# Kernel optimization log

Measured on AMD Instinct MI355X. Metric: run time of the kernel, lower is better.

The kernel has to match this reference:

```python
import jax, jax.numpy as jnp
import numpy as np

DIM = 256
WIN = (2, 7, 7)
NH = 8
BW = 2048  # num_windows * batch
N_TOK = WIN[0] * WIN[1] * WIN[2]  # 98


def _rel_coords_table():
    # Swin-V2 continuous log-spaced relative coordinates table, flattened to [T, 3]
    d = np.arange(-(WIN[0] - 1), WIN[0], dtype=np.float32)
    h = np.arange(-(WIN[1] - 1), WIN[1], dtype=np.float32)
    w = np.arange(-(WIN[2] - 1), WIN[2], dtype=np.float32)
    g = np.stack(np.meshgrid(d, h, w, indexing='ij'), axis=-1)  # [2Wd-1, 2Wh-1, 2Ww-1, 3]
    eps = 1e-6
    g[..., 0] /= WIN[0] - (1 - eps)
    g[..., 1] /= WIN[1] - (1 - eps)
    g[..., 2] /= WIN[2] - (1 - eps)
    g *= 8.0
    g = np.sign(g) * np.log2(np.abs(g) + 1.0) / np.log2(8.0)
    return g.reshape(-1, 3).astype(np.float32)


def _rel_pos_index():
    # integer relative position index [N, N] into the flattened table
    coords = np.stack(np.meshgrid(np.arange(WIN[0]), np.arange(WIN[1]), np.arange(WIN[2]), indexing='ij'))
    cf = coords.reshape(3, -1)
    rc = (cf[:, :, None] - cf[:, None, :]).transpose(1, 2, 0)
    rc[..., 0] += WIN[0] - 1
    rc[..., 1] += WIN[1] - 1
    rc[..., 2] += WIN[2] - 1
    rc[..., 0] *= (2 * WIN[1] - 1) * (2 * WIN[2] - 1)
    rc[..., 1] *= 2 * WIN[2] - 1
    return rc.sum(-1).astype(np.int32)  # [N, N]


def setup_inputs() -> dict:
    key = jax.random.key(0)
    ks = jax.random.split(key, 6)
    x = jax.random.normal(ks[0], (BW, N_TOK, DIM), dtype=jnp.float32)
    qkv_w = jax.random.normal(ks[1], (3 * DIM, DIM), dtype=jnp.float32) * 0.02
    q_bias = jnp.zeros((DIM,), dtype=jnp.float32)
    v_bias = jnp.zeros((DIM,), dtype=jnp.float32)
    logit_scale = jnp.log(10.0) * jnp.ones((NH, 1, 1), dtype=jnp.float32)
    cpb_w1 = jax.random.normal(ks[2], (512, 3), dtype=jnp.float32) * 0.02
    cpb_b1 = jnp.zeros((512,), dtype=jnp.float32)
    cpb_w2 = jax.random.normal(ks[3], (NH, 512), dtype=jnp.float32) * 0.02
    proj_w = jax.random.normal(ks[4], (DIM, DIM), dtype=jnp.float32) * 0.02
    proj_b = jnp.zeros((DIM,), dtype=jnp.float32)
    return {"x": x, "qkv_w": qkv_w, "q_bias": q_bias, "v_bias": v_bias,
            "logit_scale": logit_scale, "cpb_w1": cpb_w1, "cpb_b1": cpb_b1,
            "cpb_w2": cpb_w2, "proj_w": proj_w, "proj_b": proj_b}


def reference(x, qkv_w, q_bias, v_bias, logit_scale, cpb_w1, cpb_b1, cpb_w2, proj_w, proj_b):
    B_, N, C = x.shape
    hd = C // NH
    # qkv with separate q/v biases and zero k bias (Swin-V2)
    bias = jnp.concatenate([q_bias, jnp.zeros_like(q_bias), v_bias])
    qkv = (x @ qkv_w.T + bias).reshape(B_, N, 3, NH, hd).transpose(2, 0, 3, 1, 4)
    q, k, v = qkv[0], qkv[1], qkv[2]  # each [B_, NH, N, hd]
    # cosine attention: L2-normalize q, k (F.normalize eps=1e-12)
    qn = q / jnp.maximum(jnp.linalg.norm(q, axis=-1, keepdims=True), 1e-12)
    kn = k / jnp.maximum(jnp.linalg.norm(k, axis=-1, keepdims=True), 1e-12)
    attn = jnp.einsum('bhnd,bhmd->bhnm', qn, kn)
    scale = jnp.exp(jnp.minimum(logit_scale, jnp.log(jnp.float32(100.0))))  # clamp at log(1/0.01)
    attn = attn * scale  # [NH,1,1] broadcasts
    # continuous relative position bias via cpb MLP
    table = jnp.asarray(_rel_coords_table())                     # [T, 3]
    bt = jax.nn.relu(table @ cpb_w1.T + cpb_b1) @ cpb_w2.T       # [T, NH]
    idx = jnp.asarray(_rel_pos_index().reshape(-1))              # [N*N]
    rpb = bt[idx].reshape(N, N, NH).transpose(2, 0, 1)           # [NH, N, N]
    rpb = 16.0 * jax.nn.sigmoid(rpb)
    attn = jax.nn.softmax(attn + rpb[None], axis=-1)
    out = jnp.einsum('bhnm,bhmd->bhnd', attn, v).transpose(0, 2, 1, 3).reshape(B_, N, C)
    return out @ proj_w.T + proj_b
```

## Files before the change

kernel.cpp:

```cpp
#include <hip/hip_runtime.h>
#include <math.h>

typedef _Float16 f16;
typedef _Float16 f16x4 __attribute__((ext_vector_type(4)));
typedef _Float16 f16x8 __attribute__((ext_vector_type(8)));
typedef float f32x4 __attribute__((ext_vector_type(4)));

#define NTOK 98
#define BWIN 2048

#define OFF_BT    0u
#define OFF_RPB   (1u<<20)
#define OFF_WQKV  (2u<<20)
#define OFF_WPROJ (3u<<20)
#define OFF_Q     (4u<<20)
#define QKV_SZ    (2048u*8u*98u*32u*2u)
#define OFF_K     (OFF_Q + QKV_SZ)
#define OFF_V     (OFF_K + QKV_SZ)
#define OFF_AV    (OFF_V + QKV_SZ)

__device__ __forceinline__ void gload16(const f16* g, f16* l) {
  __builtin_amdgcn_global_load_lds(
      (const __attribute__((address_space(1))) void*)g,
      (__attribute__((address_space(3))) void*)l, 16, 0, 0);
}
__device__ __forceinline__ void gload16f(const float* g, float* l) {
  __builtin_amdgcn_global_load_lds(
      (const __attribute__((address_space(1))) void*)g,
      (__attribute__((address_space(3))) void*)l, 16, 0, 0);
}

__global__ void prep_bt(const float* __restrict__ w1, const float* __restrict__ b1,
                        const float* __restrict__ w2, float* __restrict__ bt) {
  int t = blockIdx.x;
  int lane = threadIdx.x;
  int a = t / 169, rem = t % 169, b = rem / 13, c = rem % 13;
  float g0 = ((float)(a - 1) / 1.000001f) * 8.0f;
  float g1 = ((float)(b - 6) / 6.000001f) * 8.0f;
  float g2 = ((float)(c - 6) / 6.000001f) * 8.0f;
  float t0 = log2f(fabsf(g0) + 1.0f) / 3.0f; t0 = (g0 < 0.f) ? -t0 : t0;
  float t1 = log2f(fabsf(g1) + 1.0f) / 3.0f; t1 = (g1 < 0.f) ? -t1 : t1;
  float t2 = log2f(fabsf(g2) + 1.0f) / 3.0f; t2 = (g2 < 0.f) ? -t2 : t2;
  float part[8] = {0.f,0.f,0.f,0.f,0.f,0.f,0.f,0.f};
#pragma unroll
  for (int jj = 0; jj < 8; jj++) {
    int j = lane * 8 + jj;
    float hv = t0 * w1[j*3] + t1 * w1[j*3+1] + t2 * w1[j*3+2] + b1[j];
    hv = fmaxf(hv, 0.f);
#pragma unroll
    for (int h = 0; h < 8; h++) part[h] += hv * w2[h*512 + j];
  }
#pragma unroll
  for (int m = 1; m < 64; m <<= 1)
#pragma unroll
    for (int h = 0; h < 8; h++) part[h] += __shfl_xor(part[h], m);
  if (lane == 0)
#pragma unroll
    for (int h = 0; h < 8; h++) bt[t*8 + h] = part[h];
}

__global__ void prep_rpb(const float* __restrict__ bt, float* __restrict__ rpb) {
  int bid = blockIdx.x;
  int h = bid / 98, i = bid % 98;
  int j = threadIdx.x;
  if (j >= 112) return;
  float v = 0.f;
  if (j < 98) {
    int di = i / 49, hi = (i % 49) / 7, wi = i % 7;
    int dj = j / 49, hj = (j % 49) / 7, wj = j % 7;
    int idx = (di - dj + 1) * 169 + (hi - hj + 6) * 13 + (wi - wj + 6);
    float t = bt[idx*8 + h];
    v = 16.0f / (1.0f + expf(-t));
  }
  rpb[(h*98 + i)*112 + j] = v;
}

__global__ void prep_wt(const float* __restrict__ qkv_w, const float* __restrict__ proj_w,
                        f16* __restrict__ wq, f16* __restrict__ wp) {
  int t = blockIdx.x * 256 + threadIdx.x;
  wq[t] = (f16)qkv_w[t];
  if (t < 256*256) wp[t] = (f16)proj_w[t];
}

__global__ __launch_bounds__(256) void qkv_gemm(
    const float* __restrict__ x, const f16* __restrict__ wq,
    const float* __restrict__ q_bias, const float* __restrict__ v_bias,
    f16* __restrict__ qw, f16* __restrict__ kw, f16* __restrict__ vw) {
  __shared__ float Af0[128*32];
  __shared__ float Af1[128*32];
  __shared__ f16   Bf0[128*32];
  __shared__ f16   Bf1[128*32];
  int tid = threadIdx.x;
  int w = tid >> 6, lane = tid & 63, q4 = lane >> 4, l15 = lane & 15;

  int bid = blockIdx.x;
  int sid = (bid & 7) * 1176 + (bid >> 3);
  int n_t = sid % 6, m_t = sid / 6;
  int m0 = m_t * 128, n0 = n_t * 128;

  f32x4 acc[2][8] = {};

#define QSTAGE(AB, BB, KS)                                                     \
  {                                                                            \
    _Pragma("unroll")                                                          \
    for (int p = 0; p < 4; p++) {                                              \
      int e0 = p*256 + (w << 6);                                               \
      int e  = e0 + lane;                                                      \
      int r  = e >> 3, kc = e & 7;                                             \
      int kc2 = kc ^ ((r & 3) << 1);                                           \
      gload16f(x + (size_t)(m0 + r)*256 + (KS)*32 + kc2*4, &AB[e0*4]);         \
    }                                                                          \
    _Pragma("unroll")                                                          \
    for (int p = 0; p < 2; p++) {                                              \
      int e0 = p*256 + (w << 6);                                               \
      int e  = e0 + lane;                                                      \
      int r  = e >> 2, kc = e & 3;                                             \
      gload16(wq + (size_t)(n0 + r)*256 + (KS)*32 + kc*8, &BB[e0*8]);          \
    }                                                                          \
  }

#define QCOMPUTE(AB, BB)                                                       \
  {                                                                            \
    f16x8 af[2], bf[8];                                                        \
    _Pragma("unroll")                                                          \
    for (int mt = 0; mt < 2; mt++) {                                           \
      int row = w*32 + mt*16 + l15;                                            \
      int co = ((q4 ^ (row & 3)) << 3);                                        \
      f32x4 a0 = *(const f32x4*)(&AB[row*32 + co]);                            \
      f32x4 a1 = *(const f32x4*)(&AB[row*32 + co + 4]);                        \
      f16x8 v;                                                                 \
      v[0]=(f16)a0[0]; v[1]=(f16)a0[1]; v[2]=(f16)a0[2]; v[3]=(f16)a0[3];      \
      v[4]=(f16)a1[0]; v[5]=(f16)a1[1]; v[6]=(f16)a1[2]; v[7]=(f16)a1[3];      \
      af[mt] = v;                                                              \
    }                                                                          \
    _Pragma("unroll")                                                          \
    for (int nt = 0; nt < 8; nt++)                                             \
      bf[nt] = *(const f16x8*)(&BB[(nt*16 + l15)*32 + q4*8]);                  \
    _Pragma("unroll")                                                          \
    for (int mt = 0; mt < 2; mt++)                                             \
      _Pragma("unroll")                                                        \
      for (int nt = 0; nt < 8; nt++)                                           \
        acc[mt][nt] = __builtin_amdgcn_mfma_f32_16x16x32_f16(af[mt], bf[nt], acc[mt][nt], 0, 0, 0); \
  }

  QSTAGE(Af0, Bf0, 0)
  __syncthreads();
#pragma unroll
  for (int ks = 0; ks < 8; ks += 2) {
    QSTAGE(Af1, Bf1, ks + 1)
    QCOMPUTE(Af0, Bf0)
    __syncthreads();
    if (ks + 2 < 8) QSTAGE(Af0, Bf0, ks + 2)
    QCOMPUTE(Af1, Bf1)
    __syncthreads();
  }
#undef QSTAGE
#undef QCOMPUTE

  int s = n_t >> 1;
  f16* dst = (s == 0) ? qw : ((s == 1) ? kw : vw);
#pragma unroll
  for (int mt = 0; mt < 2; mt++)
#pragma unroll
    for (int nt = 0; nt < 8; nt++) {
      int c = n0 + nt*16 + l15;
      int hcol = (c >> 5) & 7, d = c & 31;
      float bias = (s == 0) ? q_bias[c & 255] : ((s == 2) ? v_bias[c & 255] : 0.0f);
#pragma unroll
      for (int r = 0; r < 4; r++) {
        int m = m0 + w*32 + mt*16 + q4*4 + r;
        int b = m / 98, tok = m % 98;
        dst[((size_t)(b*8 + hcol)*98 + tok)*32 + d] = (f16)(acc[mt][nt][r] + bias);
      }
    }
}

#define P_STR 136
__global__ __launch_bounds__(256) void attn_kernel(
    const f16* __restrict__ qw, const f16* __restrict__ kw, const f16* __restrict__ vw,
    const float* __restrict__ rpb, const float* __restrict__ logit_scale,
    f16* __restrict__ av) {
  __shared__ f16 Ps[4*16*P_STR];

  int tid = threadIdx.x;
  int wv = tid >> 6, lane = tid & 63, q4 = lane >> 4, l15 = lane & 15;
  int pair = blockIdx.x * 4 + wv;
  int b = pair >> 3, h = pair & 7;
  float scale = __expf(fminf(logit_scale[h], 4.6051701859880914f));
  const f16* qg = qw + ((size_t)pair) * (98*32);
  const f16* kg = kw + ((size_t)pair) * (98*32);
  const f16* vg = vw + ((size_t)pair) * (98*32);
  f16* pbuf = &Ps[wv * 16 * P_STR];

  {
    int r = lane >> 2, c0 = 112 + (lane & 3) * 4;
    *(ushort4*)(&pbuf[r*P_STR + c0]) = ushort4{0,0,0,0};
  }

  f16x8 kf[7];
#pragma unroll
  for (int nt = 0; nt < 7; nt++) {
    int row = nt*16 + l15; if (row > 97) row = 97;
    f16x8 raw = *(const f16x8*)(kg + row*32 + q4*8);
    float ss = 0.f;
#pragma unroll
    for (int j = 0; j < 8; j++) { float v = (float)raw[j]; ss = fmaf(v, v, ss); }
    ss += __shfl_xor(ss, 16);
    ss += __shfl_xor(ss, 32);
    float inv = 1.0f / fmaxf(sqrtf(ss), 1e-12f);
#pragma unroll
    for (int j = 0; j < 8; j++) kf[nt][j] = (f16)((float)raw[j] * inv);
  }

  f16x8 vf[2][4];
#pragma unroll
  for (int n = 0; n < 2; n++)
#pragma unroll
    for (int kt = 0; kt < 4; kt++)
#pragma unroll
      for (int j = 0; j < 8; j++) {
        int tok = kt*32 + q4*8 + j; if (tok > 97) tok = 97;
        vf[n][kt][j] = vg[tok*32 + n*16 + l15];
      }

  const float* rpb_h = rpb + (size_t)h * 98 * 112;

  for (int mt = 0; mt < 7; mt++) {
    int qrow = mt*16 + l15;
    int qcl = (qrow > 97) ? 97 : qrow;
    bool qv = qrow < 98;
    f16x8 qraw = *(const f16x8*)(qg + qcl*32 + q4*8);
    float ss = 0.f;
#pragma unroll
    for (int j = 0; j < 8; j++) { float v = (float)qraw[j]; ss = fmaf(v, v, ss); }
    ss += __shfl_xor(ss, 16);
    ss += __shfl_xor(ss, 32);
    float qinv = 1.0f / fmaxf(sqrtf(ss), 1e-12f);
    f16x8 aq;
#pragma unroll
    for (int j = 0; j < 8; j++) aq[j] = (f16)((float)qraw[j] * qinv);

    f32x4 lg[7];
    __builtin_amdgcn_s_setprio(1);
#pragma unroll
    for (int nt = 0; nt < 7; nt++) {
      f32x4 z = {0.f,0.f,0.f,0.f};
      lg[nt] = __builtin_amdgcn_mfma_f32_16x16x32_f16(kf[nt], aq, z, 0, 0, 0);
    }
    __builtin_amdgcn_s_setprio(0);

    float mrow = -1e30f;
#pragma unroll
    for (int nt = 0; nt < 7; nt++) {
      float4 rp = *(const float4*)(rpb_h + (size_t)qcl*112 + nt*16 + q4*4);
#pragma unroll
      for (int r = 0; r < 4; r++) {
        int k = nt*16 + q4*4 + r;
        float rv = (r == 0) ? rp.x : (r == 1) ? rp.y : (r == 2) ? rp.z : rp.w;
        float lv = (qv && k < 98) ? fmaf(scale, lg[nt][r], rv) : -1e30f;
        lg[nt][r] = lv;
        mrow = fmaxf(mrow, lv);
      }
    }
    mrow = fmaxf(mrow, __shfl_xor(mrow, 16));
    mrow = fmaxf(mrow, __shfl_xor(mrow, 32));
    float s = 0.f;
#pragma unroll
    for (int nt = 0; nt < 7; nt++)
#pragma unroll
      for (int r = 0; r < 4; r++) {
        float p = __expf(lg[nt][r] - mrow);
        lg[nt][r] = p;
        s += p;
      }
    s += __shfl_xor(s, 16);
    s += __shfl_xor(s, 32);
    float inv = 1.0f / s;
#pragma unroll
    for (int nt = 0; nt < 7; nt++) {
      f16x4 pv;
#pragma unroll
      for (int r = 0; r < 4; r++) pv[r] = (f16)(lg[nt][r] * inv);
      *(f16x4*)(&pbuf[l15*P_STR + nt*16 + q4*4]) = pv;
    }
    f16x8 pf[4];
#pragma unroll
    for (int kt = 0; kt < 4; kt++)
      pf[kt] = *(const f16x8*)(&pbuf[l15*P_STR + kt*32 + q4*8]);
    __builtin_amdgcn_s_setprio(1);
    f32x4 oacc[2];
#pragma unroll
    for (int n = 0; n < 2; n++) {
      f32x4 acc = {0.f,0.f,0.f,0.f};
#pragma unroll
      for (int kt = 0; kt < 4; kt++)
        acc = __builtin_amdgcn_mfma_f32_16x16x32_f16(pf[kt], vf[n][kt], acc, 0, 0, 0);
      oacc[n] = acc;
    }
    __builtin_amdgcn_s_setprio(0);
#pragma unroll
    for (int n = 0; n < 2; n++) {
      int d = n*16 + l15;
#pragma unroll
      for (int r = 0; r < 4; r++) {
        int row = mt*16 + q4*4 + r;
        if (row < 98)
          av[((size_t)(b*98 + row))*256 + h*32 + d] = (f16)oacc[n][r];
      }
    }
  }
}

__global__ __launch_bounds__(256) void proj_gemm(
    const f16* __restrict__ avi, const f16* __restrict__ wp,
    const float* __restrict__ pb, float* __restrict__ out) {
  __shared__ f16 Ap0[128*32];
  __shared__ f16 Ap1[128*32];
  __shared__ f16 Bp0[128*32];
  __shared__ f16 Bp1[128*32];
  int tid = threadIdx.x;
  int w = tid >> 6, lane = tid & 63, q4 = lane >> 4, l15 = lane & 15;

  int bid = blockIdx.x;
  int sid = (bid & 7) * 392 + (bid >> 3);
  int n_t = sid & 1, m_t = sid >> 1;
  int m0 = m_t * 128, n0 = n_t * 128;

  f32x4 acc[2][8] = {};

#define PSTAGE(AB, BB, KS)                                                     \
  {                                                                            \
    _Pragma("unroll")                                                          \
    for (int p = 0; p < 2; p++) {                                              \
      int e0 = p*256 + (w << 6);                                               \
      int e  = e0 + lane;                                                      \
      int r  = e >> 2, kc = e & 3;                                             \
      gload16(avi + (size_t)(m0 + r)*256 + (KS)*32 + kc*8, &AB[e0*8]);         \
      gload16(wp  + (size_t)(n0 + r)*256 + (KS)*32 + kc*8, &BB[e0*8]);         \
    }                                                                          \
  }

#define PCOMPUTE(AB, BB)                                                       \
  {                                                                            \
    f16x8 af[2], bf[8];                                                        \
    _Pragma("unroll")                                                          \
    for (int mt = 0; mt < 2; mt++)                                             \
      af[mt] = *(const f16x8*)(&AB[(w*32 + mt*16 + l15)*32 + q4*8]);           \
    _Pragma("unroll")                                                          \
    for (int nt = 0; nt < 8; nt++)                                             \
      bf[nt] = *(const f16x8*)(&BB[(nt*16 + l15)*32 + q4*8]);                  \
    _Pragma("unroll")                                                          \
    for (int mt = 0; mt < 2; mt++)                                             \
      _Pragma("unroll")                                                        \
      for (int nt = 0; nt < 8; nt++)                                           \
        acc[mt][nt] = __builtin_amdgcn_mfma_f32_16x16x32_f16(af[mt], bf[nt], acc[mt][nt], 0, 0, 0); \
  }

  PSTAGE(Ap0, Bp0, 0)
  __syncthreads();
#pragma unroll
  for (int ks = 0; ks < 8; ks += 2) {
    PSTAGE(Ap1, Bp1, ks + 1)
    PCOMPUTE(Ap0, Bp0)
    __syncthreads();
    if (ks + 2 < 8) PSTAGE(Ap0, Bp0, ks + 2)
    PCOMPUTE(Ap1, Bp1)
    __syncthreads();
  }
#undef PSTAGE
#undef PCOMPUTE

#pragma unroll
  for (int mt = 0; mt < 2; mt++)
#pragma unroll
    for (int nt = 0; nt < 8; nt++) {
      int c = n0 + nt*16 + l15;
      float bias = pb[c];
#pragma unroll
      for (int r = 0; r < 4; r++) {
        int m = m0 + w*32 + mt*16 + q4*4 + r;
        out[(size_t)m*256 + c] = acc[mt][nt][r] + bias;
      }
    }
}

extern "C" void kernel_launch(void* const* d_in, const int* in_sizes, int n_in,
                              void* d_out, int out_size, void* d_ws, size_t ws_size,
                              hipStream_t stream) {
  const float* x           = (const float*)d_in[0];
  const float* qkv_w       = (const float*)d_in[1];
  const float* q_bias      = (const float*)d_in[2];
  const float* v_bias      = (const float*)d_in[3];
  const float* logit_scale = (const float*)d_in[4];
  const float* cpb_w1      = (const float*)d_in[5];
  const float* cpb_b1      = (const float*)d_in[6];
  const float* cpb_w2      = (const float*)d_in[7];
  const float* proj_w      = (const float*)d_in[8];
  const float* proj_b      = (const float*)d_in[9];
  char* ws = (char*)d_ws;
  float* bt  = (float*)(ws + OFF_BT);
  float* rpb = (float*)(ws + OFF_RPB);
  f16* wq    = (f16*)(ws + OFF_WQKV);
  f16* wp    = (f16*)(ws + OFF_WPROJ);
  f16* qws   = (f16*)(ws + OFF_Q);
  f16* kws   = (f16*)(ws + OFF_K);
  f16* vws   = (f16*)(ws + OFF_V);
  f16* avs   = (f16*)(ws + OFF_AV);
  float* out = (float*)d_out;

  prep_bt<<<dim3(507), dim3(64), 0, stream>>>(cpb_w1, cpb_b1, cpb_w2, bt);
  prep_rpb<<<dim3(784), dim3(128), 0, stream>>>(bt, rpb);
  prep_wt<<<dim3(768), dim3(256), 0, stream>>>(qkv_w, proj_w, wq, wp);
  qkv_gemm<<<dim3(9408), dim3(256), 0, stream>>>(x, wq, q_bias, v_bias, qws, kws, vws);
  attn_kernel<<<dim3(4096), dim3(256), 0, stream>>>(qws, kws, vws, rpb, logit_scale, avs);
  proj_gemm<<<dim3(3136), dim3(256), 0, stream>>>(avs, wp, proj_b, out);
}
```

Baseline: 781.1 us.

## Triple-buffer LDS stages in QKV and projection GEMMs with explicit vmcnt waits

```diff
diff --git a/kernel.cpp b/kernel.cpp
--- a/kernel.cpp
+++ b/kernel.cpp
@@ -29,6 +29,9 @@
       (const __attribute__((address_space(1))) void*)g,
       (__attribute__((address_space(3))) void*)l, 16, 0, 0);
 }
+
+#define VMCNT(n) asm volatile("s_waitcnt vmcnt(" #n ")" ::: "memory")
+#define BAR() __builtin_amdgcn_s_barrier()
 
 __global__ void prep_bt(const float* __restrict__ w1, const float* __restrict__ b1,
                         const float* __restrict__ w2, float* __restrict__ bt) {
@@ -88,6 +91,7 @@
     f16* __restrict__ qw, f16* __restrict__ kw, f16* __restrict__ vw) {
   __shared__ float Af0[128*32];
   __shared__ float Af1[128*32];
+  __shared__ float Af2[128*32];
   __shared__ f16   Bf0[128*32];
   __shared__ f16   Bf1[128*32];
   int tid = threadIdx.x;
@@ -100,7 +104,7 @@
 
   f32x4 acc[2][8] = {};
 
-#define QSTAGE(AB, BB, KS)                                                     \
+#define QSTAGE_A(AB, KS)                                                       \
   {                                                                            \
     _Pragma("unroll")                                                          \
     for (int p = 0; p < 4; p++) {                                              \
@@ -110,6 +114,9 @@
       int kc2 = kc ^ ((r & 3) << 1);                                           \
       gload16f(x + (size_t)(m0 + r)*256 + (KS)*32 + kc2*4, &AB[e0*4]);         \
     }                                                                          \
+  }
+#define QSTAGE_B(BB, KS)                                                       \
+  {                                                                            \
     _Pragma("unroll")                                                          \
     for (int p = 0; p < 2; p++) {                                              \
       int e0 = p*256 + (w << 6);                                               \
@@ -119,7 +126,7 @@
     }                                                                          \
   }
 
-#define QCOMPUTE(AB, BB)                                                       \
+#define QPHASE(AB, BB, ...)                                                    \
   {                                                                            \
     f16x8 af[2], bf[8];                                                        \
     _Pragma("unroll")                                                          \
@@ -128,34 +135,44 @@
       int co = ((q4 ^ (row & 3)) << 3);                                        \
       f32x4 a0 = *(const f32x4*)(&AB[row*32 + co]);                            \
       f32x4 a1 = *(const f32x4*)(&AB[row*32 + co + 4]);                        \
-      f16x8 v;                                                                 \
-      v[0]=(f16)a0[0]; v[1]=(f16)a0[1]; v[2]=(f16)a0[2]; v[3]=(f16)a0[3];      \
-      v[4]=(f16)a1[0]; v[5]=(f16)a1[1]; v[6]=(f16)a1[2]; v[7]=(f16)a1[3];      \
-      af[mt] = v;                                                              \
+      f16x8 vv;                                                                \
+      vv[0]=(f16)a0[0]; vv[1]=(f16)a0[1]; vv[2]=(f16)a0[2]; vv[3]=(f16)a0[3];  \
+      vv[4]=(f16)a1[0]; vv[5]=(f16)a1[1]; vv[6]=(f16)a1[2]; vv[7]=(f16)a1[3];  \
+      af[mt] = vv;                                                             \
     }                                                                          \
     _Pragma("unroll")                                                          \
     for (int nt = 0; nt < 8; nt++)                                             \
       bf[nt] = *(const f16x8*)(&BB[(nt*16 + l15)*32 + q4*8]);                  \
+    __VA_ARGS__;                                                               \
+    __builtin_amdgcn_s_setprio(1);                                             \
     _Pragma("unroll")                                                          \
     for (int mt = 0; mt < 2; mt++)                                             \
       _Pragma("unroll")                                                        \
       for (int nt = 0; nt < 8; nt++)                                           \
         acc[mt][nt] = __builtin_amdgcn_mfma_f32_16x16x32_f16(af[mt], bf[nt], acc[mt][nt], 0, 0, 0); \
-  }
-
-  QSTAGE(Af0, Bf0, 0)
-  __syncthreads();
-#pragma unroll
-  for (int ks = 0; ks < 8; ks += 2) {
-    QSTAGE(Af1, Bf1, ks + 1)
-    QCOMPUTE(Af0, Bf0)
-    __syncthreads();
-    if (ks + 2 < 8) QSTAGE(Af0, Bf0, ks + 2)
-    QCOMPUTE(Af1, Bf1)
-    __syncthreads();
-  }
-#undef QSTAGE
-#undef QCOMPUTE
+    __builtin_amdgcn_s_setprio(0);                                             \
+  }
+
+  QSTAGE_A(Af0, 0) QSTAGE_B(Bf0, 0) QSTAGE_A(Af1, 1)
+  VMCNT(4); BAR();
+  QPHASE(Af0, Bf0, QSTAGE_B(Bf1, 1) QSTAGE_A(Af2, 2))
+  VMCNT(4); BAR();
+  QPHASE(Af1, Bf1, QSTAGE_B(Bf0, 2) QSTAGE_A(Af0, 3))
+  VMCNT(4); BAR();
+  QPHASE(Af2, Bf0, QSTAGE_B(Bf1, 3) QSTAGE_A(Af1, 4))
+  VMCNT(4); BAR();
+  QPHASE(Af0, Bf1, QSTAGE_B(Bf0, 4) QSTAGE_A(Af2, 5))
+  VMCNT(4); BAR();
+  QPHASE(Af1, Bf0, QSTAGE_B(Bf1, 5) QSTAGE_A(Af0, 6))
+  VMCNT(4); BAR();
+  QPHASE(Af2, Bf1, QSTAGE_B(Bf0, 6) QSTAGE_A(Af1, 7))
+  VMCNT(4); BAR();
+  QPHASE(Af0, Bf0, QSTAGE_B(Bf1, 7))
+  VMCNT(0); BAR();
+  QPHASE(Af1, Bf1, )
+#undef QSTAGE_A
+#undef QSTAGE_B
+#undef QPHASE
 
   int s = n_t >> 1;
   f16* dst = (s == 0) ? qw : ((s == 1) ? kw : vw);
@@ -316,8 +333,10 @@
     const float* __restrict__ pb, float* __restrict__ out) {
   __shared__ f16 Ap0[128*32];
   __shared__ f16 Ap1[128*32];
+  __shared__ f16 Ap2[128*32];
   __shared__ f16 Bp0[128*32];
   __shared__ f16 Bp1[128*32];
+  __shared__ f16 Bp2[128*32];
   int tid = threadIdx.x;
   int w = tid >> 6, lane = tid & 63, q4 = lane >> 4, l15 = lane & 15;
 
@@ -340,7 +359,7 @@
     }                                                                          \
   }
 
-#define PCOMPUTE(AB, BB)                                                       \
+#define PPHASE(AB, BB, ...)                                                    \
   {                                                                            \
     f16x8 af[2], bf[8];                                                        \
     _Pragma("unroll")                                                          \
@@ -349,26 +368,35 @@
     _Pragma("unroll")                                                          \
     for (int nt = 0; nt < 8; nt++)                                             \
       bf[nt] = *(const f16x8*)(&BB[(nt*16 + l15)*32 + q4*8]);                  \
+    __VA_ARGS__;                                                               \
+    __builtin_amdgcn_s_setprio(1);                                             \
     _Pragma("unroll")                                                          \
     for (int mt = 0; mt < 2; mt++)                                             \
       _Pragma("unroll")                                                        \
       for (int nt = 0; nt < 8; nt++)                                           \
         acc[mt][nt] = __builtin_amdgcn_mfma_f32_16x16x32_f16(af[mt], bf[nt], acc[mt][nt], 0, 0, 0); \
-  }
-
-  PSTAGE(Ap0, Bp0, 0)
-  __syncthreads();
-#pragma unroll
-  for (int ks = 0; ks < 8; ks += 2) {
-    PSTAGE(Ap1, Bp1, ks + 1)
-    PCOMPUTE(Ap0, Bp0)
-    __syncthreads();
-    if (ks + 2 < 8) PSTAGE(Ap0, Bp0, ks + 2)
-    PCOMPUTE(Ap1, Bp1)
-    __syncthreads();
-  }
+    __builtin_amdgcn_s_setprio(0);                                             \
+  }
+
+  PSTAGE(Ap0, Bp0, 0) PSTAGE(Ap1, Bp1, 1)
+  VMCNT(4); BAR();
+  PPHASE(Ap0, Bp0, PSTAGE(Ap2, Bp2, 2))
+  VMCNT(4); BAR();
+  PPHASE(Ap1, Bp1, PSTAGE(Ap0, Bp0, 3))
+  VMCNT(4); BAR();
+  PPHASE(Ap2, Bp2, PSTAGE(Ap1, Bp1, 4))
+  VMCNT(4); BAR();
+  PPHASE(Ap0, Bp0, PSTAGE(Ap2, Bp2, 5))
+  VMCNT(4); BAR();
+  PPHASE(Ap1, Bp1, PSTAGE(Ap0, Bp0, 6))
+  VMCNT(4); BAR();
+  PPHASE(Ap2, Bp2, PSTAGE(Ap1, Bp1, 7))
+  VMCNT(4); BAR();
+  PPHASE(Ap0, Bp0, )
+  VMCNT(0); BAR();
+  PPHASE(Ap1, Bp1, )
 #undef PSTAGE
-#undef PCOMPUTE
+#undef PPHASE
 
 #pragma unroll
   for (int mt = 0; mt < 2; mt++)
```

Result: slower. 808.7 us (+3.5%).
